# Optimization experiments

Measured on AMD Instinct MI355X. Metric: run time of the kernel, lower is better.

The kernel has to match this reference:

```python
import jax, jax.numpy as jnp
import numpy as np

N_FFT = 2048
HOP = 441
WIN_SIZE = 7
PAD = WIN_SIZE // 2
NP_WIN = WIN_SIZE * WIN_SIZE
COV_NORM = NP_WIN / (NP_WIN - 1.0)  # sample covariance, skimage default
DATA_RANGE = 2.0  # skimage float dtype_range (-1,1)
C1 = (0.01 * DATA_RANGE) ** 2
C2 = (0.03 * DATA_RANGE) ** 2
EPS = 1e-8

# periodic hann window (librosa fftbins=True)
_HANN = 0.5 - 0.5 * np.cos(2.0 * np.pi * np.arange(N_FFT) / N_FFT)


def wav_to_spectrogram(x):
    # x: [B, C, S] -> magnitude spectrogram [B, C, T, F]
    pad = N_FFT // 2
    xp = jnp.pad(x, ((0, 0), (0, 0), (pad, pad)), mode='reflect')  # torch 'reflect'
    L = xp.shape[-1]
    n_frames = (L - N_FFT) // HOP + 1
    idx = jnp.arange(n_frames)[:, None] * HOP + jnp.arange(N_FFT)[None, :]
    frames = xp[..., idx] * jnp.asarray(_HANN, xp.dtype)  # [B,C,T,N_FFT]
    spec = jnp.fft.rfft(frames, axis=-1)
    mag = jnp.sqrt(jnp.maximum(spec.real ** 2 + spec.imag ** 2, EPS))
    return mag


def _umean_last(x):
    # 1D uniform mean filter (size 7) along last axis, scipy 'reflect' boundary
    xp = jnp.pad(x, [(0, 0)] * (x.ndim - 1) + [(PAD, PAD)], mode='symmetric')
    cs = jnp.cumsum(xp, axis=-1)
    zero = jnp.zeros(cs.shape[:-1] + (1,), cs.dtype)
    cs = jnp.concatenate([zero, cs], axis=-1)
    return (cs[..., WIN_SIZE:] - cs[..., :-WIN_SIZE]) / WIN_SIZE


def umean2d(x):
    # separable 7x7 uniform filter over last two axes
    x = _umean_last(x)
    x = jnp.swapaxes(_umean_last(jnp.swapaxes(x, -1, -2)), -1, -2)
    return x


def ssim_map_mean(X, Y):
    ux, uy = umean2d(X), umean2d(Y)
    uxx, uyy, uxy = umean2d(X * X), umean2d(Y * Y), umean2d(X * Y)
    vx = COV_NORM * (uxx - ux * ux)
    vy = COV_NORM * (uyy - uy * uy)
    vxy = COV_NORM * (uxy - ux * uy)
    S = ((2 * ux * uy + C1) * (2 * vxy + C2)) / ((ux * ux + uy * uy + C1) * (vx + vy + C2))
    # crop pad on each side (skimage) then mean over the spatial map
    return jnp.mean(S[..., PAD:-PAD, PAD:-PAD], axis=(-2, -1))


def setup_inputs() -> dict:
    key = jax.random.key(0)
    k1, k2 = jax.random.split(key)
    B, C, S = 32, 2, 176400
    output = jax.random.normal(k1, (B, C, S), dtype=jnp.float32)
    target = jax.random.normal(k2, (B, C, S), dtype=jnp.float32)
    return {"output": output, "target": target}


def reference(output, target):
    so = wav_to_spectrogram(output)
    st = wav_to_spectrogram(target)
    res = ssim_map_mean(so, st)  # [B, C]
    return res[..., None, None]  # [B, C, 1, 1]
```

## Files before the change

kernel.cpp:

```cpp
#include <hip/hip_runtime.h>
#include <math.h>

#ifndef M_PI
#define M_PI 3.14159265358979323846
#endif

constexpr int S_LEN    = 176400;
constexpr int NFFT     = 2048;
constexpr int NC       = 1024;
constexpr int HOP_     = 441;
constexpr int T_FRAMES = 401;
constexpr int F_BINS   = 1025;
constexpr int F_STRIDE = 1028;
constexpr int N_CH     = 64;
constexpr float EPS_   = 1e-8f;
constexpr float C1_    = 0.0004f;
constexpr float C2_    = 0.0036f;
constexpr float COV_NORM_ = 49.0f / 48.0f;

constexpr int WIN_OFF  = 0;
constexpr int TWG_OFF  = 2048;
constexpr int UTW_OFF  = 3584;
constexpr int SPEC_OFF = 5696;
constexpr int RPB_     = 10;
constexpr int N_CHUNKS = 40;

__device__ __forceinline__ int phys(int i) { return i ^ ((i >> 2) & 15); }

__device__ __forceinline__ float2 cadd(float2 a, float2 b){ return make_float2(a.x+b.x, a.y+b.y); }
__device__ __forceinline__ float2 csub(float2 a, float2 b){ return make_float2(a.x-b.x, a.y-b.y); }
__device__ __forceinline__ float2 cmul(float2 a, float2 b){ return make_float2(a.x*b.x-a.y*b.y, a.x*b.y+a.y*b.x); }

__global__ __launch_bounds__(256) void init_tables_kernel(float* __restrict__ ws, float* __restrict__ out) {
    const int idx = blockIdx.x * 256 + threadIdx.x;
    if (idx < 64) out[idx] = 0.0f;
    if (idx < NFFT) {
        ws[WIN_OFF + idx] = 0.5f - 0.5f * cosf((float)(2.0 * M_PI / NFFT) * (float)idx);
    }
    if (idx < 768) {
        float ang = -2.0f * (float)M_PI * (float)idx / (float)NC;
        float s, c; sincosf(ang, &s, &c);
        ws[TWG_OFF + 2*idx] = c; ws[TWG_OFF + 2*idx+1] = s;
    }
    if (idx < F_BINS) {
        float ang = -(float)M_PI * (float)idx / (float)NC;
        float s, c; sincosf(ang, &s, &c);
        ws[UTW_OFF + 2*idx] = c; ws[UTW_OFF + 2*idx+1] = s;
    }
}

__global__ __launch_bounds__(256, 8) void stft_mag_kernel(
    const float* __restrict__ x0, const float* __restrict__ x1,
    float* __restrict__ ws, int ch0, int nch, int swizzle)
{
    __shared__ float2 bufA[NC];
    __shared__ float2 bufB[NC];

    const int tid = threadIdx.x;

    int ch, which, t;
    if (swizzle) {
        int g = blockIdx.x;
        ch    = ch0 + (g & 7) * 8 + ((g >> 3) & 7);
        which = (g >> 6) & 1;
        t     = g >> 7;
    } else {
        int bx = blockIdx.x;
        which = bx / T_FRAMES;
        t     = bx - which * T_FRAMES;
        ch    = ch0 + blockIdx.y;
    }

    const float* __restrict__ xin = (which ? x1 : x0) + (size_t)ch * S_LEN;
    const float*  __restrict__ win = ws + WIN_OFF;
    const float2* __restrict__ twg = (const float2*)(ws + TWG_OFF);
    const float2* __restrict__ utw = (const float2*)(ws + UTW_OFF);

    const int base = t * HOP_ - NFFT / 2;
    float* bufAf = (float*)bufA;
    #pragma unroll
    for (int k = 0; k < NFFT / 256; ++k) {
        int n = k * 256 + tid;
        int j = base + n;
        j = (j < 0) ? -j : j;
        j = (j >= S_LEN) ? (2 * S_LEN - 2 - j) : j;
        float v = xin[j] * win[n];
        int ci = n >> 1;
        bufAf[2 * phys(ci) + (n & 1)] = v;
    }
    __syncthreads();

    float2* A = bufA;
    float2* B = bufB;
    #pragma unroll
    for (int i = 0; i < 5; ++i) {
        const int s_ = 1 << (2 * i);
        const int q  = tid & (s_ - 1);
        const int ps = tid - q;

        float2 x0c = A[phys(tid)];
        float2 x1c = A[phys(tid + 256)];
        float2 x2c = A[phys(tid + 512)];
        float2 x3c = A[phys(tid + 768)];

        float2 t0 = cadd(x0c, x2c);
        float2 t1 = csub(x0c, x2c);
        float2 t2 = cadd(x1c, x3c);
        float2 t3 = csub(x1c, x3c);

        float2 y0 = cadd(t0, t2);
        float2 y2 = csub(t0, t2);
        float2 y1 = make_float2(t1.x + t3.y, t1.y - t3.x);
        float2 y3 = make_float2(t1.x - t3.y, t1.y + t3.x);

        float2 w1 = twg[ps];
        float2 w2 = twg[2 * ps];
        float2 w3 = twg[3 * ps];

        float2 z1 = cmul(y1, w1);
        float2 z2 = cmul(y2, w2);
        float2 z3 = cmul(y3, w3);

        const int o = q + 4 * ps;
        B[phys(o)]          = y0;
        B[phys(o + s_)]     = z1;
        B[phys(o + 2 * s_)] = z2;
        B[phys(o + 3 * s_)] = z3;
        __syncthreads();
        float2* tmp = A; A = B; B = tmp;
    }

    float* __restrict__ sout =
        ws + SPEC_OFF + ((size_t)which * nch + (size_t)(ch - ch0)) * (size_t)T_FRAMES * F_STRIDE
                      + (size_t)t * F_STRIDE;
    #pragma unroll
    for (int k = 0; k < 5; ++k) {
        int r = k * 256 + tid;
        if (k < 4 || tid == 0) {
            float2 Zr = A[phys(r & (NC - 1))];
            float2 Zn = A[phys((NC - r) & (NC - 1))];
            float Ex = 0.5f * (Zr.x + Zn.x);
            float Ey = 0.5f * (Zr.y - Zn.y);
            float Ox = 0.5f * (Zr.y + Zn.y);
            float Oy = 0.5f * (Zn.x - Zr.x);
            float2 wu = utw[r];
            float Xx = Ex + wu.x * Ox - wu.y * Oy;
            float Xy = Ey + wu.x * Oy + wu.y * Ox;
            sout[r] = sqrtf(fmaxf(Xx * Xx + Xy * Xy, EPS_));
        }
    }
}

__global__ __launch_bounds__(256) void ssim_kernel(
    const float* __restrict__ ws, float* __restrict__ out,
    int ch0, int nch)
{
    __shared__ float csx[1284], csy[1284], csxx[1284], csyy[1284], csxy[1284];
    __shared__ double red[256];

    const int tid = threadIdx.x;
    const int cg  = blockIdx.y;
    const int ch  = ch0 + cg;
    const float* __restrict__ spec = ws + SPEC_OFF;
    const size_t per_ch = (size_t)T_FRAMES * F_STRIDE;
    const float* __restrict__ X = spec + (size_t)cg * per_ch;
    const float* __restrict__ Y = spec + ((size_t)nch + cg) * per_ch;

    const int t_begin = 3 + blockIdx.x * RPB_;
    const int t_end_  = min(t_begin + RPB_, T_FRAMES - 3);

    const int fv = tid << 2;
    const bool last = (tid == 255);
    const float inv49 = 1.0f / 49.0f;
    double acc = 0.0;

    float sx[4] = {0,0,0,0}, sy[4] = {0,0,0,0}, sxx[4] = {0,0,0,0},
          syy[4] = {0,0,0,0}, sxy[4] = {0,0,0,0};
    float s5[5] = {0,0,0,0,0};

    for (int rr = t_begin - 3; rr < t_begin + 3; ++rr) {
        float4 xv = *(const float4*)(X + (size_t)rr * F_STRIDE + fv);
        float4 yv = *(const float4*)(Y + (size_t)rr * F_STRIDE + fv);
        float xa[4] = {xv.x, xv.y, xv.z, xv.w}, ya[4] = {yv.x, yv.y, yv.z, yv.w};
        #pragma unroll
        for (int c = 0; c < 4; ++c) {
            sx[c] += xa[c]; sy[c] += ya[c];
            sxx[c] += xa[c]*xa[c]; syy[c] += ya[c]*ya[c]; sxy[c] += xa[c]*ya[c];
        }
        if (last) {
            float xe = X[(size_t)rr * F_STRIDE + 1024];
            float ye = Y[(size_t)rr * F_STRIDE + 1024];
            s5[0] += xe; s5[1] += ye; s5[2] += xe*xe; s5[3] += ye*ye; s5[4] += xe*ye;
        }
    }

    float4 ax, ay, bx, by; float a5x=0, a5y=0, b5x=0, b5y=0;
    ax = *(const float4*)(X + (size_t)(t_begin + 3) * F_STRIDE + fv);
    ay = *(const float4*)(Y + (size_t)(t_begin + 3) * F_STRIDE + fv);
    bx = *(const float4*)(X + (size_t)(t_begin - 3) * F_STRIDE + fv);
    by = *(const float4*)(Y + (size_t)(t_begin - 3) * F_STRIDE + fv);
    if (last) {
        a5x = X[(size_t)(t_begin + 3) * F_STRIDE + 1024];
        a5y = Y[(size_t)(t_begin + 3) * F_STRIDE + 1024];
        b5x = X[(size_t)(t_begin - 3) * F_STRIDE + 1024];
        b5y = Y[(size_t)(t_begin - 3) * F_STRIDE + 1024];
    }

    const int fo = 3 + (tid << 2);

    for (int t = t_begin; t < t_end_; ++t) {
        {
            float xa[4] = {ax.x, ax.y, ax.z, ax.w}, ya[4] = {ay.x, ay.y, ay.z, ay.w};
            #pragma unroll
            for (int c = 0; c < 4; ++c) {
                sx[c] += xa[c]; sy[c] += ya[c];
                sxx[c] += xa[c]*xa[c]; syy[c] += ya[c]*ya[c]; sxy[c] += xa[c]*ya[c];
                int p = 5 * tid + c;
                csx[p] = sx[c]; csy[p] = sy[c];
                csxx[p] = sxx[c]; csyy[p] = syy[c]; csxy[p] = sxy[c];
            }
            if (last) {
                s5[0] += a5x; s5[1] += a5y; s5[2] += a5x*a5x; s5[3] += a5y*a5y; s5[4] += a5x*a5y;
                csx[1280] = s5[0]; csy[1280] = s5[1];
                csxx[1280] = s5[2]; csyy[1280] = s5[3]; csxy[1280] = s5[4];
            }
        }
        __syncthreads();

        {
            float xa[4] = {bx.x, bx.y, bx.z, bx.w}, ya[4] = {by.x, by.y, by.z, by.w};
            #pragma unroll
            for (int c = 0; c < 4; ++c) {
                sx[c] -= xa[c]; sy[c] -= ya[c];
                sxx[c] -= xa[c]*xa[c]; syy[c] -= ya[c]*ya[c]; sxy[c] -= xa[c]*ya[c];
            }
            if (last) {
                s5[0] -= b5x; s5[1] -= b5y; s5[2] -= b5x*b5x; s5[3] -= b5y*b5y; s5[4] -= b5x*b5y;
            }
        }
        if (t + 1 < t_end_) {
            ax = *(const float4*)(X + (size_t)(t + 4) * F_STRIDE + fv);
            ay = *(const float4*)(Y + (size_t)(t + 4) * F_STRIDE + fv);
            bx = *(const float4*)(X + (size_t)(t - 2) * F_STRIDE + fv);
            by = *(const float4*)(Y + (size_t)(t - 2) * F_STRIDE + fv);
            if (last) {
                a5x = X[(size_t)(t + 4) * F_STRIDE + 1024];
                a5y = Y[(size_t)(t + 4) * F_STRIDE + 1024];
                b5x = X[(size_t)(t - 2) * F_STRIDE + 1024];
                b5y = Y[(size_t)(t - 2) * F_STRIDE + 1024];
            }
        }

        if (tid < 255) {
            float tx[10], ty[10], txx[10], tyy[10], txy[10];
            #pragma unroll
            for (int d = 0; d < 10; ++d) {
                int p = 5 * tid + d + (d >> 2);
                tx[d] = csx[p]; ty[d] = csy[p];
                txx[d] = csxx[p]; tyy[d] = csyy[p]; txy[d] = csxy[p];
            }
            float wx  = tx[0]+tx[1]+tx[2]+tx[3]+tx[4]+tx[5]+tx[6];
            float wy  = ty[0]+ty[1]+ty[2]+ty[3]+ty[4]+ty[5]+ty[6];
            float wxx = txx[0]+txx[1]+txx[2]+txx[3]+txx[4]+txx[5]+txx[6];
            float wyy = tyy[0]+tyy[1]+tyy[2]+tyy[3]+tyy[4]+tyy[5]+tyy[6];
            float wxy = txy[0]+txy[1]+txy[2]+txy[3]+txy[4]+txy[5]+txy[6];
            #pragma unroll
            for (int c = 0; c < 4; ++c) {
                if (fo + c <= 1021) {
                    float ux  = wx * inv49, uy  = wy * inv49;
                    float uxx = wxx * inv49, uyy = wyy * inv49, uxy = wxy * inv49;
                    float vx  = COV_NORM_ * (uxx - ux * ux);
                    float vy  = COV_NORM_ * (uyy - uy * uy);
                    float vxy = COV_NORM_ * (uxy - ux * uy);
                    float Sv = ((2.f * ux * uy + C1_) * (2.f * vxy + C2_)) /
                               ((ux * ux + uy * uy + C1_) * (vx + vy + C2_));
                    acc += (double)Sv;
                }
                if (c < 3) {
                    wx  += tx[c+7]  - tx[c];
                    wy  += ty[c+7]  - ty[c];
                    wxx += txx[c+7] - txx[c];
                    wyy += tyy[c+7] - tyy[c];
                    wxy += txy[c+7] - txy[c];
                }
            }
        }
        __syncthreads();
    }

    red[tid] = acc;
    __syncthreads();
    for (int off = 128; off > 0; off >>= 1) {
        if (tid < off) red[tid] += red[tid + off];
        __syncthreads();
    }
    if (tid == 0) {
        atomicAdd(&out[ch], (float)(red[0] / (395.0 * 1019.0)));
    }
}

extern "C" void kernel_launch(void* const* d_in, const int* in_sizes, int n_in,
                              void* d_out, int out_size, void* d_ws, size_t ws_size,
                              hipStream_t stream) {
    const float* x0 = (const float*)d_in[0];
    const float* x1 = (const float*)d_in[1];
    float* out = (float*)d_out;
    float* ws  = (float*)d_ws;

    const size_t table_bytes  = (size_t)SPEC_OFF * sizeof(float);
    const size_t per_ch_bytes = (size_t)2 * T_FRAMES * F_STRIDE * sizeof(float);
    int G = (int)((ws_size - table_bytes) / per_ch_bytes);
    if (G > N_CH) G = N_CH;
    if (G < 1)    G = 1;

    init_tables_kernel<<<dim3(16), dim3(256), 0, stream>>>(ws, out);

    for (int ch0 = 0; ch0 < N_CH; ch0 += G) {
        const int nch = (N_CH - ch0 < G) ? (N_CH - ch0) : G;

        if (nch == 64) {
            stft_mag_kernel<<<dim3(T_FRAMES * 128), dim3(256), 0, stream>>>(x0, x1, ws, ch0, nch, 1);
        } else {
            stft_mag_kernel<<<dim3(2 * T_FRAMES, nch), dim3(256), 0, stream>>>(x0, x1, ws, ch0, nch, 0);
        }

        dim3 g2(N_CHUNKS, nch);
        ssim_kernel<<<g2, 256, 0, stream>>>(ws, out, ch0, nch);
    }
}
```

Baseline: 368.6 us.

## Process both output and target frames per STFT block with shared twiddles

Each STFT block now computes the FFT of the same frame for both input signals, doubling shared memory buffers and halving the grid. Twiddle and index computations are shared across the two butterflies, and the window value is loaded once per sample. A fast path skips reflect-boundary index arithmetic for interior frames. Occupancy hint drops from 8 to 5 blocks per CU because shared memory per block doubles.

```diff
diff --git a/kernel.cpp b/kernel.cpp
--- a/kernel.cpp
+++ b/kernel.cpp
@@ -49,44 +49,83 @@
     }
 }
 
-__global__ __launch_bounds__(256, 8) void stft_mag_kernel(
+__device__ __forceinline__ void r4_bfly(
+    const float2* __restrict__ A, float2* __restrict__ B,
+    int r0, int r1, int r2, int r3,
+    int o0, int o1, int o2, int o3,
+    float2 w1, float2 w2, float2 w3)
+{
+    float2 x0c = A[r0];
+    float2 x1c = A[r1];
+    float2 x2c = A[r2];
+    float2 x3c = A[r3];
+
+    float2 t0 = cadd(x0c, x2c);
+    float2 t1 = csub(x0c, x2c);
+    float2 t2 = cadd(x1c, x3c);
+    float2 t3 = csub(x1c, x3c);
+
+    float2 y0 = cadd(t0, t2);
+    float2 y2 = csub(t0, t2);
+    float2 y1 = make_float2(t1.x + t3.y, t1.y - t3.x);
+    float2 y3 = make_float2(t1.x - t3.y, t1.y + t3.x);
+
+    B[o0] = y0;
+    B[o1] = cmul(y1, w1);
+    B[o2] = cmul(y2, w2);
+    B[o3] = cmul(y3, w3);
+}
+
+__global__ __launch_bounds__(256, 5) void stft_mag_kernel(
     const float* __restrict__ x0, const float* __restrict__ x1,
     float* __restrict__ ws, int ch0, int nch, int swizzle)
 {
-    __shared__ float2 bufA[NC];
-    __shared__ float2 bufB[NC];
+    __shared__ float2 bufA[2 * NC];
+    __shared__ float2 bufB[2 * NC];
 
     const int tid = threadIdx.x;
 
-    int ch, which, t;
+    int ch, t;
     if (swizzle) {
         int g = blockIdx.x;
-        ch    = ch0 + (g & 7) * 8 + ((g >> 3) & 7);
-        which = (g >> 6) & 1;
-        t     = g >> 7;
+        ch = ch0 + (g & 7) * 8 + ((g >> 3) & 7);
+        t  = g >> 6;
     } else {
-        int bx = blockIdx.x;
-        which = bx / T_FRAMES;
-        t     = bx - which * T_FRAMES;
-        ch    = ch0 + blockIdx.y;
-    }
-
-    const float* __restrict__ xin = (which ? x1 : x0) + (size_t)ch * S_LEN;
+        t  = blockIdx.x;
+        ch = ch0 + blockIdx.y;
+    }
+
+    const float* __restrict__ xin0 = x0 + (size_t)ch * S_LEN;
+    const float* __restrict__ xin1 = x1 + (size_t)ch * S_LEN;
     const float*  __restrict__ win = ws + WIN_OFF;
     const float2* __restrict__ twg = (const float2*)(ws + TWG_OFF);
     const float2* __restrict__ utw = (const float2*)(ws + UTW_OFF);
 
     const int base = t * HOP_ - NFFT / 2;
-    float* bufAf = (float*)bufA;
-    #pragma unroll
-    for (int k = 0; k < NFFT / 256; ++k) {
-        int n = k * 256 + tid;
-        int j = base + n;
-        j = (j < 0) ? -j : j;
-        j = (j >= S_LEN) ? (2 * S_LEN - 2 - j) : j;
-        float v = xin[j] * win[n];
-        int ci = n >> 1;
-        bufAf[2 * phys(ci) + (n & 1)] = v;
+    float* fA0 = (float*)bufA;
+    float* fA1 = (float*)(bufA + NC);
+    if (base >= 0 && base + NFFT <= S_LEN) {
+        #pragma unroll
+        for (int k = 0; k < NFFT / 256; ++k) {
+            int n = k * 256 + tid;
+            int j = base + n;
+            float w = win[n];
+            int p = 2 * phys(n >> 1) + (n & 1);
+            fA0[p] = xin0[j] * w;
+            fA1[p] = xin1[j] * w;
+        }
+    } else {
+        #pragma unroll
+        for (int k = 0; k < NFFT / 256; ++k) {
+            int n = k * 256 + tid;
+            int j = base + n;
+            j = (j < 0) ? -j : j;
+            j = (j >= S_LEN) ? (2 * S_LEN - 2 - j) : j;
+            float w = win[n];
+            int p = 2 * phys(n >> 1) + (n & 1);
+            fA0[p] = xin0[j] * w;
+            fA1[p] = xin1[j] * w;
+        }
     }
     __syncthreads();
 
@@ -98,55 +137,62 @@
         const int q  = tid & (s_ - 1);
         const int ps = tid - q;
 
-        float2 x0c = A[phys(tid)];
-        float2 x1c = A[phys(tid + 256)];
-        float2 x2c = A[phys(tid + 512)];
-        float2 x3c = A[phys(tid + 768)];
-
-        float2 t0 = cadd(x0c, x2c);
-        float2 t1 = csub(x0c, x2c);
-        float2 t2 = cadd(x1c, x3c);
-        float2 t3 = csub(x1c, x3c);
-
-        float2 y0 = cadd(t0, t2);
-        float2 y2 = csub(t0, t2);
-        float2 y1 = make_float2(t1.x + t3.y, t1.y - t3.x);
-        float2 y3 = make_float2(t1.x - t3.y, t1.y + t3.x);
-
-        float2 w1 = twg[ps];
-        float2 w2 = twg[2 * ps];
-        float2 w3 = twg[3 * ps];
-
-        float2 z1 = cmul(y1, w1);
-        float2 z2 = cmul(y2, w2);
-        float2 z3 = cmul(y3, w3);
-
-        const int o = q + 4 * ps;
-        B[phys(o)]          = y0;
-        B[phys(o + s_)]     = z1;
-        B[phys(o + 2 * s_)] = z2;
-        B[phys(o + 3 * s_)] = z3;
+        const int r0 = phys(tid);
+        const int r1 = phys(tid + 256);
+        const int r2 = phys(tid + 512);
+        const int r3 = phys(tid + 768);
+
+        const float2 w1 = twg[ps];
+        const float2 w2 = twg[2 * ps];
+        const float2 w3 = twg[3 * ps];
+
+        const int o  = q + 4 * ps;
+        const int o0 = phys(o);
+        const int o1 = phys(o + s_);
+        const int o2 = phys(o + 2 * s_);
+        const int o3 = phys(o + 3 * s_);
+
+        r4_bfly(A,      B,      r0, r1, r2, r3, o0, o1, o2, o3, w1, w2, w3);
+        r4_bfly(A + NC, B + NC, r0, r1, r2, r3, o0, o1, o2, o3, w1, w2, w3);
+
         __syncthreads();
         float2* tmp = A; A = B; B = tmp;
     }
 
-    float* __restrict__ sout =
-        ws + SPEC_OFF + ((size_t)which * nch + (size_t)(ch - ch0)) * (size_t)T_FRAMES * F_STRIDE
-                      + (size_t)t * F_STRIDE;
+    const size_t perT = (size_t)T_FRAMES * F_STRIDE;
+    float* __restrict__ sout0 =
+        ws + SPEC_OFF + (size_t)(ch - ch0) * perT + (size_t)t * F_STRIDE;
+    float* __restrict__ sout1 = sout0 + (size_t)nch * perT;
     #pragma unroll
     for (int k = 0; k < 5; ++k) {
         int r = k * 256 + tid;
         if (k < 4 || tid == 0) {
-            float2 Zr = A[phys(r & (NC - 1))];
-            float2 Zn = A[phys((NC - r) & (NC - 1))];
-            float Ex = 0.5f * (Zr.x + Zn.x);
-            float Ey = 0.5f * (Zr.y - Zn.y);
-            float Ox = 0.5f * (Zr.y + Zn.y);
-            float Oy = 0.5f * (Zn.x - Zr.x);
+            const int ra = phys(r & (NC - 1));
+            const int rb = phys((NC - r) & (NC - 1));
             float2 wu = utw[r];
-            float Xx = Ex + wu.x * Ox - wu.y * Oy;
-            float Xy = Ey + wu.x * Oy + wu.y * Ox;
-            sout[r] = sqrtf(fmaxf(Xx * Xx + Xy * Xy, EPS_));
+
+            {
+                float2 Zr = A[ra];
+                float2 Zn = A[rb];
+                float Ex = 0.5f * (Zr.x + Zn.x);
+                float Ey = 0.5f * (Zr.y - Zn.y);
+                float Ox = 0.5f * (Zr.y + Zn.y);
+                float Oy = 0.5f * (Zn.x - Zr.x);
+                float Xx = Ex + wu.x * Ox - wu.y * Oy;
+                float Xy = Ey + wu.x * Oy + wu.y * Ox;
+                sout0[r] = sqrtf(fmaxf(Xx * Xx + Xy * Xy, EPS_));
+            }
+            {
+                float2 Zr = A[NC + ra];
+                float2 Zn = A[NC + rb];
+                float Ex = 0.5f * (Zr.x + Zn.x);
+                float Ey = 0.5f * (Zr.y - Zn.y);
+                float Ox = 0.5f * (Zr.y + Zn.y);
+                float Oy = 0.5f * (Zn.x - Zr.x);
+                float Xx = Ex + wu.x * Ox - wu.y * Oy;
+                float Xy = Ey + wu.x * Oy + wu.y * Ox;
+                sout1[r] = sqrtf(fmaxf(Xx * Xx + Xy * Xy, EPS_));
+            }
         }
     }
 }
@@ -319,9 +365,9 @@
         const int nch = (N_CH - ch0 < G) ? (N_CH - ch0) : G;
 
         if (nch == 64) {
-            stft_mag_kernel<<<dim3(T_FRAMES * 128), dim3(256), 0, stream>>>(x0, x1, ws, ch0, nch, 1);
+            stft_mag_kernel<<<dim3(T_FRAMES * 64), dim3(256), 0, stream>>>(x0, x1, ws, ch0, nch, 1);
         } else {
-            stft_mag_kernel<<<dim3(2 * T_FRAMES, nch), dim3(256), 0, stream>>>(x0, x1, ws, ch0, nch, 0);
+            stft_mag_kernel<<<dim3(T_FRAMES, nch), dim3(256), 0, stream>>>(x0, x1, ws, ch0, nch, 0);
         }
 
         dim3 g2(N_CHUNKS, nch);
```

Result: no change. 365.3 us (-0.9%).
